# Kernel tuning notes

Hardware: AMD Instinct MI355X
Metric: run time of the kernel (lower is better)

The kernel has to match this reference:

```python
import jax, jax.numpy as jnp
import numpy as np

N_NODES = 10000
N_EDGES = 160000
F_IN, D1, D2, D_OUT, K = 512, 512, 512, 256, 3


def _gcn_layer(x, row, col, w, W, b, n):
    # PyG GCNConv (improved=False): add self-loops with weight 1, sym norm.
    loop = jnp.arange(n)
    r = jnp.concatenate([row, loop])
    c = jnp.concatenate([col, loop])
    ww = jnp.concatenate([w, jnp.ones((n,), w.dtype)])
    deg = jax.ops.segment_sum(ww, c, num_segments=n)
    dinv = jnp.where(deg > 0, jax.lax.rsqrt(deg), 0.0)
    norm = dinv[r] * ww * dinv[c]              # [E+N]
    h = x @ W                                  # dense GEMM first (as PyG lin)
    out = jax.ops.segment_sum(norm[:, None] * h[r], c, num_segments=n)
    return out + b


def _cheb_layer(x, row, col, w, Wk, b, n):
    # PyG ChebConv, normalization='sym', lambda_max=2.0:
    # L_hat = 2L/lmax - I = -D^{-1/2} A D^{-1/2} (self-loops removed first).
    w0 = jnp.where(row == col, jnp.zeros((), w.dtype), w)  # remove self loops
    deg = jax.ops.segment_sum(w0, row, num_segments=n)
    dinv = jnp.where(deg > 0, jax.lax.rsqrt(deg), 0.0)
    norm = dinv[row] * w0 * dinv[col]          # [E]

    def lhat(z):  # L_hat @ z
        return -jax.ops.segment_sum(norm[:, None] * z[row], col, num_segments=n)

    Tx0 = x
    out = Tx0 @ Wk[0]
    Tx1 = lhat(x)
    out = out + Tx1 @ Wk[1]
    for k in range(2, Wk.shape[0]):            # static K, fine to unroll
        Tx2 = 2.0 * lhat(Tx1) - Tx0
        out = out + Tx2 @ Wk[k]
        Tx0, Tx1 = Tx1, Tx2
    return out + b


def setup_inputs() -> dict:
    key = jax.random.key(0)
    ks = jax.random.split(key, 9)
    x = jax.random.normal(ks[0], (N_NODES, F_IN), dtype=jnp.float32)
    edge_index = jax.random.randint(ks[1], (2, N_EDGES), 0, N_NODES, dtype=jnp.int64)
    edge_weight = jax.random.uniform(ks[2], (N_EDGES,), dtype=jnp.float32)
    s = lambda fan: 1.0 / np.sqrt(fan)
    W1 = jax.random.normal(ks[3], (F_IN, D1), dtype=jnp.float32) * s(F_IN)
    b1 = jnp.zeros((D1,), jnp.float32)
    W2 = jax.random.normal(ks[4], (D1, D2), dtype=jnp.float32) * s(D1)
    b2 = jnp.zeros((D2,), jnp.float32)
    Wc = jax.random.normal(ks[5], (K, D2, D_OUT), dtype=jnp.float32) * s(D2)
    bc = jnp.zeros((D_OUT,), jnp.float32)
    return {"x": x, "edge_index": edge_index, "edge_weight": edge_weight,
            "W1": W1, "b1": b1, "W2": W2, "b2": b2, "Wc": Wc, "bc": bc}


def reference(x, edge_index, edge_weight, W1, b1, W2, b2, Wc, bc):
    row, col = edge_index[0], edge_index[1]
    n = x.shape[0]
    h = jax.nn.celu(_gcn_layer(x, row, col, edge_weight, W1, b1, n))
    h = jax.nn.celu(_gcn_layer(h, row, col, edge_weight, W2, b2, n))
    h = jax.nn.celu(_cheb_layer(h, row, col, edge_weight, Wc, bc, n))
    return h
```

## Files before the change

### kernel.cpp

```cpp
#include <hip/hip_runtime.h>
#include <math.h>

#define N_NODES 10000
#define N_EDGES 160000
#define FDIM    512
#define DOUT    256
#define NCAT    768

typedef unsigned short ushort_t;
typedef unsigned int   uint_t;
typedef __attribute__((ext_vector_type(8))) short bf16x8;
typedef __attribute__((ext_vector_type(4))) float f32x4;

__device__ inline ushort_t f2bf(float f) {
    uint_t u = __float_as_uint(f);
    u += 0x7fffu + ((u >> 16) & 1u);
    return (ushort_t)(u >> 16);
}
__device__ inline void bf2f8(uint4 u, float* v) {
    v[0] = __uint_as_float(u.x << 16); v[1] = __uint_as_float(u.x & 0xffff0000u);
    v[2] = __uint_as_float(u.y << 16); v[3] = __uint_as_float(u.y & 0xffff0000u);
    v[4] = __uint_as_float(u.z << 16); v[5] = __uint_as_float(u.z & 0xffff0000u);
    v[6] = __uint_as_float(u.w << 16); v[7] = __uint_as_float(u.w & 0xffff0000u);
}
__device__ inline uint4 f2bf8v(const float* v) {
    uint4 u;
    u.x = (uint_t)f2bf(v[0]) | ((uint_t)f2bf(v[1]) << 16);
    u.y = (uint_t)f2bf(v[2]) | ((uint_t)f2bf(v[3]) << 16);
    u.z = (uint_t)f2bf(v[4]) | ((uint_t)f2bf(v[5]) << 16);
    u.w = (uint_t)f2bf(v[6]) | ((uint_t)f2bf(v[7]) << 16);
    return u;
}
__device__ inline void gld_lds16(const ushort_t* g, ushort_t* l) {
    __builtin_amdgcn_global_load_lds(
        (const __attribute__((address_space(1))) unsigned int*)g,
        (__attribute__((address_space(3))) unsigned int*)l,
        16, 0, 0);
}

__global__ void k_edge_deg(const int* __restrict__ row, const int* __restrict__ col,
                           const float* __restrict__ w,
                           float* deg_g, float* deg_c, int* counts, int E) {
    int e = blockIdx.x * blockDim.x + threadIdx.x;
    if (e >= E) return;
    int r = row[e], c = col[e];
    float wv = w[e];
    atomicAdd(&deg_g[c], wv);
    if (r != c) atomicAdd(&deg_c[r], wv);
    atomicAdd(&counts[c], 1);
}

__global__ __launch_bounds__(256) void k_dinv_scan1(
    const float* __restrict__ deg_g, const float* __restrict__ deg_c,
    float* __restrict__ dinv_g, float* __restrict__ dinv_c,
    const int* __restrict__ counts, int* __restrict__ rp,
    int* __restrict__ part, int n)
{
    __shared__ int s[256];
    int tid = threadIdx.x;
    int i = blockIdx.x * 256 + tid;
    if (i < n) {
        dinv_g[i] = rsqrtf(deg_g[i] + 1.0f);
        float d = deg_c[i];
        dinv_c[i] = d > 0.f ? rsqrtf(d) : 0.f;
    }
    int v = (i < n) ? counts[i] : 0;
    s[tid] = v;
    __syncthreads();
    for (int o = 1; o < 256; o <<= 1) {
        int t = (tid >= o) ? s[tid - o] : 0;
        __syncthreads();
        s[tid] += t;
        __syncthreads();
    }
    if (i < n) rp[i] = s[tid] - v;
    if (tid == 255) part[blockIdx.x] = s[255];
}

__global__ __launch_bounds__(256) void k_scan23(int* __restrict__ rp,
                                                const int* __restrict__ part,
                                                int nb, int n) {
    __shared__ int soff[64];
    __shared__ int stot;
    int tid = threadIdx.x;
    if (tid < 64) {
        int v = (tid < nb) ? part[tid] : 0;
        int x = v;
        for (int o = 1; o < 64; o <<= 1) {
            int y = __shfl_up(x, o, 64);
            if (tid >= o) x += y;
        }
        soff[tid] = x - v;
        if (tid == 63) stot = x;
    }
    __syncthreads();
    int i = blockIdx.x * 256 + tid;
    if (i < n) rp[i] += soff[blockIdx.x];
    if (blockIdx.x == 0 && tid == 0) rp[n] = stot;
}

__global__ void k_fill(const int* __restrict__ row, const int* __restrict__ col,
                       const float* __restrict__ w,
                       const float* __restrict__ dinv_g, const float* __restrict__ dinv_c,
                       const int* __restrict__ rp, int* __restrict__ fill,
                       int2* __restrict__ eg, int2* __restrict__ ec, int E) {
    int e = blockIdx.x * blockDim.x + threadIdx.x;
    if (e >= E) return;
    int r = row[e], c = col[e];
    float wv = w[e];
    float ng = dinv_g[r] * wv * dinv_g[c];
    float w0 = (r == c) ? 0.f : wv;
    float nc = -(dinv_c[r] * w0 * dinv_c[c]);
    int pos = rp[c] + atomicAdd(&fill[c], 1);
    eg[pos] = make_int2(r, __float_as_int(ng));
    ec[pos] = make_int2(r, __float_as_int(nc));
}

#define XB_BLOCKS 5000

__global__ __launch_bounds__(256) void k_conv(
    const float* __restrict__ x,  ushort_t* __restrict__ xb,
    const float* __restrict__ W1, ushort_t* __restrict__ W1t,
    const float* __restrict__ W2, ushort_t* __restrict__ W2t,
    const float* __restrict__ Wc, ushort_t* __restrict__ Wcatt)
{
    int b = blockIdx.x;
    int tid = threadIdx.x;
    if (b < XB_BLOCKS) {
        int t = b * 256 + tid;
        float4 v = *(const float4*)(x + (size_t)t * 4);
        uint2 p;
        p.x = (uint_t)f2bf(v.x) | ((uint_t)f2bf(v.y) << 16);
        p.y = (uint_t)f2bf(v.z) | ((uint_t)f2bf(v.w) << 16);
        *(uint2*)(xb + (size_t)t * 4) = p;
        return;
    }
    b -= XB_BLOCKS;
    __shared__ float tile[64][65];
    const float* src; const float* src2 = nullptr;
    ushort_t* dst; int kt, ntG, srcld;
    if (b < 64) {
        kt = b >> 3; ntG = b & 7; srcld = FDIM;
        src = W1 + (size_t)(kt * 64) * FDIM + ntG * 64;
        dst = W1t;
    } else if (b < 128) {
        int bb = b - 64;
        kt = bb >> 3; ntG = bb & 7; srcld = FDIM;
        src = W2 + (size_t)(kt * 64) * FDIM + ntG * 64;
        dst = W2t;
    } else {
        int bb = b - 128;
        ntG = bb / 8; kt = bb % 8; srcld = DOUT;
        int s = ntG >> 2;
        int nl = (ntG & 3) * 64;
        if (s == 0) {
            src  = Wc + (size_t)(kt * 64) * DOUT + nl;
            src2 = Wc + (size_t)2 * FDIM * DOUT + (size_t)(kt * 64) * DOUT + nl;
        } else if (s == 1) {
            src  = Wc + (size_t)1 * FDIM * DOUT + (size_t)(kt * 64) * DOUT + nl;
        } else {
            src  = Wc + (size_t)2 * FDIM * DOUT + (size_t)(kt * 64) * DOUT + nl;
        }
        dst = Wcatt;
    }
    {
        int r = tid >> 2, c0 = (tid & 3) * 16;
        const float* sp = src + (size_t)r * srcld + c0;
#pragma unroll
        for (int q = 0; q < 4; ++q) {
            float4 a = *(const float4*)(sp + q * 4);
            if (src2) {
                float4 bsub = *(const float4*)(src2 + (size_t)r * srcld + c0 + q * 4);
                a.x -= bsub.x; a.y -= bsub.y; a.z -= bsub.z; a.w -= bsub.w;
            }
            tile[r][c0 + q * 4 + 0] = a.x;
            tile[r][c0 + q * 4 + 1] = a.y;
            tile[r][c0 + q * 4 + 2] = a.z;
            tile[r][c0 + q * 4 + 3] = a.w;
        }
    }
    __syncthreads();
    {
        int n = tid >> 2, k0 = (tid & 3) * 16;
        float v[16];
#pragma unroll
        for (int i = 0; i < 16; ++i) v[i] = tile[k0 + i][n];
        uint4 u0 = f2bf8v(v);
        uint4 u1 = f2bf8v(v + 8);
        ushort_t* dp = dst + (size_t)(ntG * 64 + n) * FDIM + kt * 64 + k0;
        *(uint4*)dp = u0;
        *(uint4*)(dp + 8) = u1;
    }
}

__global__ __launch_bounds__(256) void k_mgemm(
    const ushort_t* __restrict__ A, int lda,
    const ushort_t* __restrict__ Bt, int ldb,
    int M, int K, int N, int nbx, int nby,
    ushort_t* __restrict__ outB)
{
    __shared__ ushort_t As[128 * 32];
    __shared__ ushort_t Bs[128 * 32];

    int id = blockIdx.x;
    int j = id & 7, t = id >> 3;
    int by = t % nby;
    int bx = (t / nby) * 8 + j;
    if (bx >= nbx) return;

    const int tid  = threadIdx.x;
    const int w    = tid >> 6;
    const int lane = tid & 63;
    const int l15  = lane & 15;
    const int quad = lane >> 4;
    const int bm = bx * 128, bn = by * 128;
    const int wm = (w & 1) * 64;
    const int wn = (w >> 1) * 64;

    const int sr = lane >> 2;
    const int sc = (lane & 3) * 8;
    const ushort_t* ag[2]; ushort_t* al[2];
#pragma unroll
    for (int i = 0; i < 2; ++i) {
        int rt = (w * 2 + i) * 16 + sr;
        int ar = min(bm + rt, M - 1);
        ag[i] = A + (size_t)ar * lda + sc;
        al[i] = As + rt * 32 + sc;
    }
    const ushort_t* bg[2]; ushort_t* bl[2];
#pragma unroll
    for (int i = 0; i < 2; ++i) {
        int rt = (w * 2 + i) * 16 + sr;
        bg[i] = Bt + (size_t)(bn + rt) * ldb + sc;
        bl[i] = Bs + rt * 32 + sc;
    }

    f32x4 acc[4][4] = {};

    for (int k0 = 0; k0 < K; k0 += 32) {
        __syncthreads();
#pragma unroll
        for (int i = 0; i < 2; ++i) gld_lds16(ag[i] + k0, al[i]);
#pragma unroll
        for (int i = 0; i < 2; ++i) gld_lds16(bg[i] + k0, bl[i]);
        __syncthreads();
        bf16x8 af[4], bfr[4];
#pragma unroll
        for (int i = 0; i < 4; ++i)
            af[i] = *(const bf16x8*)(As + (wm + i * 16 + l15) * 32 + quad * 8);
#pragma unroll
        for (int jj = 0; jj < 4; ++jj)
            bfr[jj] = *(const bf16x8*)(Bs + (wn + jj * 16 + l15) * 32 + quad * 8);
#pragma unroll
        for (int i = 0; i < 4; ++i)
#pragma unroll
            for (int jj = 0; jj < 4; ++jj)
                acc[i][jj] = __builtin_amdgcn_mfma_f32_16x16x32_bf16(af[i], bfr[jj], acc[i][jj], 0, 0, 0);
    }

#pragma unroll
    for (int i = 0; i < 4; ++i) {
        int rowb = bm + wm + i * 16 + quad * 4;
#pragma unroll
        for (int jj = 0; jj < 4; ++jj) {
            int col = bn + wn + jj * 16 + l15;
#pragma unroll
            for (int r = 0; r < 4; ++r) {
                int rr = rowb + r;
                if (rr < M)
                    outB[(size_t)rr * N + col] = f2bf(acc[i][jj][r]);
            }
        }
    }
}

template<int SL>
__global__ __launch_bounds__(256) void k_sagg(
    const ushort_t* __restrict__ h, int hs, int hoff,
    const int2* __restrict__ er, const int* __restrict__ rp,
    const float* __restrict__ dinv_g,
    const ushort_t* __restrict__ other, int os, int ooff, float sB,
    const float* __restrict__ bias, float sA,
    ushort_t* __restrict__ outB, float* __restrict__ outF, int outs, int celu)
{
    const int id  = blockIdx.x;
    const int sl  = id % SL;
    const int tid = threadIdx.x;
    const int c   = (id / SL) * 32 + (tid >> 3);
    if (c >= N_NODES) return;
    const int f = sl * 64 + ((tid & 7) << 3);
    const ushort_t* hp = h + hoff + f;

    float acc[8] = {0.f, 0.f, 0.f, 0.f, 0.f, 0.f, 0.f, 0.f};
    int e = rp[c];
    const int e1 = rp[c + 1];
    for (; e + 2 <= e1; e += 2) {
        int2 p0 = er[e], p1 = er[e + 1];
        uint4 u0 = *(const uint4*)(hp + (size_t)p0.x * hs);
        uint4 u1 = *(const uint4*)(hp + (size_t)p1.x * hs);
        float n0 = __int_as_float(p0.y), n1 = __int_as_float(p1.y);
        float v0[8], v1[8];
        bf2f8(u0, v0); bf2f8(u1, v1);
#pragma unroll
        for (int i = 0; i < 8; ++i) {
            acc[i] = fmaf(n0, v0[i], acc[i]);
            acc[i] = fmaf(n1, v1[i], acc[i]);
        }
    }
    if (e < e1) {
        int2 p = er[e];
        uint4 u = *(const uint4*)(hp + (size_t)p.x * hs);
        float nv = __int_as_float(p.y);
        float v[8]; bf2f8(u, v);
#pragma unroll
        for (int i = 0; i < 8; ++i) acc[i] = fmaf(nv, v[i], acc[i]);
    }

    if (dinv_g) {
        float dv = dinv_g[c];
        float d2 = dv * dv;
        uint4 u = *(const uint4*)(hp + (size_t)c * hs);
        float v[8]; bf2f8(u, v);
#pragma unroll
        for (int i = 0; i < 8; ++i) acc[i] = fmaf(d2, v[i], acc[i]);
    }
    float r[8];
#pragma unroll
    for (int i = 0; i < 8; ++i) r[i] = sA * acc[i];
    if (other) {
        uint4 u = *(const uint4*)(other + (size_t)c * os + ooff + f);
        float o[8]; bf2f8(u, o);
#pragma unroll
        for (int i = 0; i < 8; ++i) r[i] = fmaf(sB, o[i], r[i]);
    }
    if (bias) {
#pragma unroll
        for (int i = 0; i < 8; ++i) r[i] += bias[f + i];
    }
    if (celu) {
#pragma unroll
        for (int i = 0; i < 8; ++i) r[i] = r[i] > 0.f ? r[i] : expm1f(r[i]);
    }
    if (outF) {
        float* op = outF + (size_t)c * outs + f;
        *(float4*)op       = make_float4(r[0], r[1], r[2], r[3]);
        *(float4*)(op + 4) = make_float4(r[4], r[5], r[6], r[7]);
    } else {
        *(uint4*)(outB + (size_t)c * outs + f) = f2bf8v(r);
    }
}


extern "C" void kernel_launch(void* const* d_in, const int* in_sizes, int n_in,
                              void* d_out, int out_size, void* d_ws, size_t ws_size,
                              hipStream_t stream) {
    const float* x  = (const float*)d_in[0];
    const int*   ei = (const int*)d_in[1];
    const float* ew = (const float*)d_in[2];
    const float* W1 = (const float*)d_in[3];
    const float* b1 = (const float*)d_in[4];
    const float* W2 = (const float*)d_in[5];
    const float* b2 = (const float*)d_in[6];
    const float* Wc = (const float*)d_in[7];
    const float* bc = (const float*)d_in[8];
    float* out = (float*)d_out;

    const int* row = ei;
    const int* col = ei + N_EDGES;

    char* ws = (char*)d_ws;
    size_t off = 0;
    auto alloc = [&](size_t bytes) -> void* {
        void* p = ws + off;
        off += (bytes + 255) & ~(size_t)255;
        return p;
    };
    ushort_t* xb    = (ushort_t*)alloc((size_t)N_NODES * FDIM * 2);
    ushort_t* bufA  = (ushort_t*)alloc((size_t)N_NODES * FDIM * 2);
    ushort_t* bufB  = (ushort_t*)alloc((size_t)N_NODES * FDIM * 2);
    ushort_t* Y     = (ushort_t*)alloc((size_t)N_NODES * NCAT * 2);
    ushort_t* P     = (ushort_t*)alloc((size_t)N_NODES * DOUT * 2);
    ushort_t* W1t   = (ushort_t*)alloc((size_t)FDIM * FDIM * 2);
    ushort_t* W2t   = (ushort_t*)alloc((size_t)FDIM * FDIM * 2);
    ushort_t* Wcatt = (ushort_t*)alloc((size_t)NCAT * FDIM * 2);
    size_t zs = off;
    float* deg_g  = (float*)alloc((size_t)N_NODES * 4);
    float* deg_c  = (float*)alloc((size_t)N_NODES * 4);
    int*   counts = (int*)alloc((size_t)N_NODES * 4);
    int*   fillb  = (int*)alloc((size_t)N_NODES * 4);
    size_t ze = off;
    float* dinv_g = (float*)alloc((size_t)N_NODES * 4);
    float* dinv_c = (float*)alloc((size_t)N_NODES * 4);
    int*   rp     = (int*)alloc((size_t)(N_NODES + 1) * 4);
    int*   part   = (int*)alloc(64 * 4);
    int2*  eg     = (int2*)alloc((size_t)N_EDGES * 8);
    int2*  ec     = (int2*)alloc((size_t)N_EDGES * 8);

    const int TB = 256;
    dim3 edgeGrid((N_EDGES + TB - 1) / TB);
    int nScanB = (N_NODES + 255) / 256;

    hipMemsetAsync(ws + zs, 0, ze - zs, stream);
    k_edge_deg<<<edgeGrid, TB, 0, stream>>>(row, col, ew, deg_g, deg_c, counts, N_EDGES);
    k_dinv_scan1<<<nScanB, 256, 0, stream>>>(deg_g, deg_c, dinv_g, dinv_c, counts, rp, part, N_NODES);
    k_scan23<<<nScanB, 256, 0, stream>>>(rp, part, nScanB, N_NODES);
    k_fill<<<edgeGrid, TB, 0, stream>>>(row, col, ew, dinv_g, dinv_c, rp, fillb, eg, ec, N_EDGES);

    k_conv<<<XB_BLOCKS + 224, 256, 0, stream>>>(x, xb, W1, W1t, W2, W2t, Wc, Wcatt);

    auto mgemm = [&](const ushort_t* A, const ushort_t* Bt, int N, ushort_t* oB) {
        int nbx = (N_NODES + 127) / 128, nby = N / 128;
        int G = 8 * (((nbx + 7) / 8) * nby);
        k_mgemm<<<G, 256, 0, stream>>>(A, FDIM, Bt, FDIM, N_NODES, FDIM, N, nbx, nby, oB);
    };
    int g8 = ((N_NODES + 31) / 32) * 8;
    int g4 = ((N_NODES + 31) / 32) * 4;

    mgemm(xb, W1t, FDIM, bufA);
    k_sagg<8><<<g8, 256, 0, stream>>>(bufA, FDIM, 0, eg, rp, dinv_g,
                                      (const ushort_t*)nullptr, 0, 0, 0.f,
                                      b1, 1.f, bufB, (float*)nullptr, FDIM, 1);
    mgemm(bufB, W2t, FDIM, bufA);
    k_sagg<8><<<g8, 256, 0, stream>>>(bufA, FDIM, 0, eg, rp, dinv_g,
                                      (const ushort_t*)nullptr, 0, 0, 0.f,
                                      b2, 1.f, bufB, (float*)nullptr, FDIM, 1);
    mgemm(bufB, Wcatt, NCAT, Y);
    k_sagg<4><<<g4, 256, 0, stream>>>(Y, NCAT, 2 * DOUT, ec, rp,
                                      (const float*)nullptr,
                                      Y, NCAT, DOUT, 1.f,
                                      (const float*)nullptr, 2.f,
                                      P, (float*)nullptr, DOUT, 0);
    k_sagg<4><<<g4, 256, 0, stream>>>(P, DOUT, 0, ec, rp,
                                      (const float*)nullptr,
                                      Y, NCAT, 0, 1.f,
                                      bc, 1.f,
                                      (ushort_t*)nullptr, out, DOUT, 1);
}
```

Baseline: 256.1 us.

## Fuse edge-degree with conversion kernel, shrink GEMM M-tile, unroll aggregation by four

The edge-degree atomics are merged into the bf16 conversion kernel, saving one launch and letting the two independent jobs overlap. The GEMM tile is reduced from 128x128 to 64x128 rows per block, which doubles the block count so the 10000-row problem fills more CUs, at the cost of less B-tile reuse. The sparse aggregation loop is unrolled to four edges per iteration to keep more gathers in flight, with a scalar remainder loop.

New measurement: 239.7 us, median of 3. 6.4% less time.

```diff
diff --git a/kernel.cpp b/kernel.cpp
--- a/kernel.cpp
+++ b/kernel.cpp
@@ -38,94 +38,33 @@
         16, 0, 0);
 }
 
-__global__ void k_edge_deg(const int* __restrict__ row, const int* __restrict__ col,
-                           const float* __restrict__ w,
-                           float* deg_g, float* deg_c, int* counts, int E) {
-    int e = blockIdx.x * blockDim.x + threadIdx.x;
-    if (e >= E) return;
-    int r = row[e], c = col[e];
-    float wv = w[e];
-    atomicAdd(&deg_g[c], wv);
-    if (r != c) atomicAdd(&deg_c[r], wv);
-    atomicAdd(&counts[c], 1);
-}
-
-__global__ __launch_bounds__(256) void k_dinv_scan1(
-    const float* __restrict__ deg_g, const float* __restrict__ deg_c,
-    float* __restrict__ dinv_g, float* __restrict__ dinv_c,
-    const int* __restrict__ counts, int* __restrict__ rp,
-    int* __restrict__ part, int n)
-{
-    __shared__ int s[256];
-    int tid = threadIdx.x;
-    int i = blockIdx.x * 256 + tid;
-    if (i < n) {
-        dinv_g[i] = rsqrtf(deg_g[i] + 1.0f);
-        float d = deg_c[i];
-        dinv_c[i] = d > 0.f ? rsqrtf(d) : 0.f;
-    }
-    int v = (i < n) ? counts[i] : 0;
-    s[tid] = v;
-    __syncthreads();
-    for (int o = 1; o < 256; o <<= 1) {
-        int t = (tid >= o) ? s[tid - o] : 0;
-        __syncthreads();
-        s[tid] += t;
-        __syncthreads();
-    }
-    if (i < n) rp[i] = s[tid] - v;
-    if (tid == 255) part[blockIdx.x] = s[255];
-}
-
-__global__ __launch_bounds__(256) void k_scan23(int* __restrict__ rp,
-                                                const int* __restrict__ part,
-                                                int nb, int n) {
-    __shared__ int soff[64];
-    __shared__ int stot;
-    int tid = threadIdx.x;
-    if (tid < 64) {
-        int v = (tid < nb) ? part[tid] : 0;
-        int x = v;
-        for (int o = 1; o < 64; o <<= 1) {
-            int y = __shfl_up(x, o, 64);
-            if (tid >= o) x += y;
-        }
-        soff[tid] = x - v;
-        if (tid == 63) stot = x;
-    }
-    __syncthreads();
-    int i = blockIdx.x * 256 + tid;
-    if (i < n) rp[i] += soff[blockIdx.x];
-    if (blockIdx.x == 0 && tid == 0) rp[n] = stot;
-}
-
-__global__ void k_fill(const int* __restrict__ row, const int* __restrict__ col,
-                       const float* __restrict__ w,
-                       const float* __restrict__ dinv_g, const float* __restrict__ dinv_c,
-                       const int* __restrict__ rp, int* __restrict__ fill,
-                       int2* __restrict__ eg, int2* __restrict__ ec, int E) {
-    int e = blockIdx.x * blockDim.x + threadIdx.x;
-    if (e >= E) return;
-    int r = row[e], c = col[e];
-    float wv = w[e];
-    float ng = dinv_g[r] * wv * dinv_g[c];
-    float w0 = (r == c) ? 0.f : wv;
-    float nc = -(dinv_c[r] * w0 * dinv_c[c]);
-    int pos = rp[c] + atomicAdd(&fill[c], 1);
-    eg[pos] = make_int2(r, __float_as_int(ng));
-    ec[pos] = make_int2(r, __float_as_int(nc));
-}
-
-#define XB_BLOCKS 5000
-
-__global__ __launch_bounds__(256) void k_conv(
+#define EDGE_BLOCKS 625
+#define XB_BLOCKS   5000
+
+__global__ __launch_bounds__(256) void k_pre1(
+    const int* __restrict__ row, const int* __restrict__ col,
+    const float* __restrict__ w,
+    float* deg_g, float* deg_c, int* counts,
     const float* __restrict__ x,  ushort_t* __restrict__ xb,
     const float* __restrict__ W1, ushort_t* __restrict__ W1t,
     const float* __restrict__ W2, ushort_t* __restrict__ W2t,
     const float* __restrict__ Wc, ushort_t* __restrict__ Wcatt)
 {
+    __shared__ float tile[64][65];
     int b = blockIdx.x;
     int tid = threadIdx.x;
+    if (b < EDGE_BLOCKS) {
+        int e = b * 256 + tid;
+        if (e < N_EDGES) {
+            int r = row[e], c = col[e];
+            float wv = w[e];
+            atomicAdd(&deg_g[c], wv);
+            if (r != c) atomicAdd(&deg_c[r], wv);
+            atomicAdd(&counts[c], 1);
+        }
+        return;
+    }
+    b -= EDGE_BLOCKS;
     if (b < XB_BLOCKS) {
         int t = b * 256 + tid;
         float4 v = *(const float4*)(x + (size_t)t * 4);
@@ -136,7 +75,6 @@
         return;
     }
     b -= XB_BLOCKS;
-    __shared__ float tile[64][65];
     const float* src; const float* src2 = nullptr;
     ushort_t* dst; int kt, ntG, srcld;
     if (b < 64) {
@@ -193,13 +131,79 @@
     }
 }
 
+__global__ __launch_bounds__(256) void k_dinv_scan1(
+    const float* __restrict__ deg_g, const float* __restrict__ deg_c,
+    float* __restrict__ dinv_g, float* __restrict__ dinv_c,
+    const int* __restrict__ counts, int* __restrict__ rp,
+    int* __restrict__ part, int n)
+{
+    __shared__ int s[256];
+    int tid = threadIdx.x;
+    int i = blockIdx.x * 256 + tid;
+    if (i < n) {
+        dinv_g[i] = rsqrtf(deg_g[i] + 1.0f);
+        float d = deg_c[i];
+        dinv_c[i] = d > 0.f ? rsqrtf(d) : 0.f;
+    }
+    int v = (i < n) ? counts[i] : 0;
+    s[tid] = v;
+    __syncthreads();
+    for (int o = 1; o < 256; o <<= 1) {
+        int t = (tid >= o) ? s[tid - o] : 0;
+        __syncthreads();
+        s[tid] += t;
+        __syncthreads();
+    }
+    if (i < n) rp[i] = s[tid] - v;
+    if (tid == 255) part[blockIdx.x] = s[255];
+}
+
+__global__ __launch_bounds__(256) void k_scan23(int* __restrict__ rp,
+                                                const int* __restrict__ part,
+                                                int nb, int n) {
+    __shared__ int soff[64];
+    __shared__ int stot;
+    int tid = threadIdx.x;
+    if (tid < 64) {
+        int v = (tid < nb) ? part[tid] : 0;
+        int x = v;
+        for (int o = 1; o < 64; o <<= 1) {
+            int y = __shfl_up(x, o, 64);
+            if (tid >= o) x += y;
+        }
+        soff[tid] = x - v;
+        if (tid == 63) stot = x;
+    }
+    __syncthreads();
+    int i = blockIdx.x * 256 + tid;
+    if (i < n) rp[i] += soff[blockIdx.x];
+    if (blockIdx.x == 0 && tid == 0) rp[n] = stot;
+}
+
+__global__ void k_fill(const int* __restrict__ row, const int* __restrict__ col,
+                       const float* __restrict__ w,
+                       const float* __restrict__ dinv_g, const float* __restrict__ dinv_c,
+                       const int* __restrict__ rp, int* __restrict__ fill,
+                       int2* __restrict__ eg, int2* __restrict__ ec, int E) {
+    int e = blockIdx.x * blockDim.x + threadIdx.x;
+    if (e >= E) return;
+    int r = row[e], c = col[e];
+    float wv = w[e];
+    float ng = dinv_g[r] * wv * dinv_g[c];
+    float w0 = (r == c) ? 0.f : wv;
+    float nc = -(dinv_c[r] * w0 * dinv_c[c]);
+    int pos = rp[c] + atomicAdd(&fill[c], 1);
+    eg[pos] = make_int2(r, __float_as_int(ng));
+    ec[pos] = make_int2(r, __float_as_int(nc));
+}
+
 __global__ __launch_bounds__(256) void k_mgemm(
     const ushort_t* __restrict__ A, int lda,
     const ushort_t* __restrict__ Bt, int ldb,
     int M, int K, int N, int nbx, int nby,
     ushort_t* __restrict__ outB)
 {
-    __shared__ ushort_t As[128 * 32];
+    __shared__ ushort_t As[64 * 32];
     __shared__ ushort_t Bs[128 * 32];
 
     int id = blockIdx.x;
@@ -213,53 +217,44 @@
     const int lane = tid & 63;
     const int l15  = lane & 15;
     const int quad = lane >> 4;
-    const int bm = bx * 128, bn = by * 128;
-    const int wm = (w & 1) * 64;
+    const int bm = bx * 64, bn = by * 128;
+    const int wm = (w & 1) * 32;
     const int wn = (w >> 1) * 64;
 
     const int sr = lane >> 2;
     const int sc = (lane & 3) * 8;
-    const ushort_t* ag[2]; ushort_t* al[2];
-#pragma unroll
-    for (int i = 0; i < 2; ++i) {
-        int rt = (w * 2 + i) * 16 + sr;
-        int ar = min(bm + rt, M - 1);
-        ag[i] = A + (size_t)ar * lda + sc;
-        al[i] = As + rt * 32 + sc;
-    }
-    const ushort_t* bg[2]; ushort_t* bl[2];
-#pragma unroll
-    for (int i = 0; i < 2; ++i) {
-        int rt = (w * 2 + i) * 16 + sr;
-        bg[i] = Bt + (size_t)(bn + rt) * ldb + sc;
-        bl[i] = Bs + rt * 32 + sc;
-    }
-
-    f32x4 acc[4][4] = {};
+    int arow = min(bm + w * 16 + sr, M - 1);
+    const ushort_t* ag = A + (size_t)arow * lda + sc;
+    ushort_t* al = As + (w * 16 + sr) * 32 + sc;
+    const ushort_t* bg0 = Bt + (size_t)(bn + w * 32 + sr) * ldb + sc;
+    const ushort_t* bg1 = bg0 + (size_t)16 * ldb;
+    ushort_t* bl0 = Bs + (w * 32 + sr) * 32 + sc;
+    ushort_t* bl1 = bl0 + 16 * 32;
+
+    f32x4 acc[2][4] = {};
 
     for (int k0 = 0; k0 < K; k0 += 32) {
         __syncthreads();
-#pragma unroll
-        for (int i = 0; i < 2; ++i) gld_lds16(ag[i] + k0, al[i]);
-#pragma unroll
-        for (int i = 0; i < 2; ++i) gld_lds16(bg[i] + k0, bl[i]);
+        gld_lds16(ag + k0, al);
+        gld_lds16(bg0 + k0, bl0);
+        gld_lds16(bg1 + k0, bl1);
         __syncthreads();
-        bf16x8 af[4], bfr[4];
-#pragma unroll
-        for (int i = 0; i < 4; ++i)
+        bf16x8 af[2], bfr[4];
+#pragma unroll
+        for (int i = 0; i < 2; ++i)
             af[i] = *(const bf16x8*)(As + (wm + i * 16 + l15) * 32 + quad * 8);
 #pragma unroll
         for (int jj = 0; jj < 4; ++jj)
             bfr[jj] = *(const bf16x8*)(Bs + (wn + jj * 16 + l15) * 32 + quad * 8);
 #pragma unroll
-        for (int i = 0; i < 4; ++i)
+        for (int i = 0; i < 2; ++i)
 #pragma unroll
             for (int jj = 0; jj < 4; ++jj)
                 acc[i][jj] = __builtin_amdgcn_mfma_f32_16x16x32_bf16(af[i], bfr[jj], acc[i][jj], 0, 0, 0);
     }
 
 #pragma unroll
-    for (int i = 0; i < 4; ++i) {
+    for (int i = 0; i < 2; ++i) {
         int rowb = bm + wm + i * 16 + quad * 4;
 #pragma unroll
         for (int jj = 0; jj < 4; ++jj) {
@@ -294,20 +289,25 @@
     float acc[8] = {0.f, 0.f, 0.f, 0.f, 0.f, 0.f, 0.f, 0.f};
     int e = rp[c];
     const int e1 = rp[c + 1];
-    for (; e + 2 <= e1; e += 2) {
-        int2 p0 = er[e], p1 = er[e + 1];
+    for (; e + 4 <= e1; e += 4) {
+        int2 p0 = er[e], p1 = er[e + 1], p2 = er[e + 2], p3 = er[e + 3];
         uint4 u0 = *(const uint4*)(hp + (size_t)p0.x * hs);
         uint4 u1 = *(const uint4*)(hp + (size_t)p1.x * hs);
+        uint4 u2 = *(const uint4*)(hp + (size_t)p2.x * hs);
+        uint4 u3 = *(const uint4*)(hp + (size_t)p3.x * hs);
         float n0 = __int_as_float(p0.y), n1 = __int_as_float(p1.y);
-        float v0[8], v1[8];
-        bf2f8(u0, v0); bf2f8(u1, v1);
+        float n2 = __int_as_float(p2.y), n3 = __int_as_float(p3.y);
+        float v0[8], v1[8], v2[8], v3[8];
+        bf2f8(u0, v0); bf2f8(u1, v1); bf2f8(u2, v2); bf2f8(u3, v3);
 #pragma unroll
         for (int i = 0; i < 8; ++i) {
             acc[i] = fmaf(n0, v0[i], acc[i]);
             acc[i] = fmaf(n1, v1[i], acc[i]);
-        }
-    }
-    if (e < e1) {
+            acc[i] = fmaf(n2, v2[i], acc[i]);
+            acc[i] = fmaf(n3, v3[i], acc[i]);
+        }
+    }
+    for (; e < e1; ++e) {
         int2 p = er[e];
         uint4 u = *(const uint4*)(hp + (size_t)p.x * hs);
         float nv = __int_as_float(p.y);
@@ -401,15 +401,15 @@
     int nScanB = (N_NODES + 255) / 256;
 
     hipMemsetAsync(ws + zs, 0, ze - zs, stream);
-    k_edge_deg<<<edgeGrid, TB, 0, stream>>>(row, col, ew, deg_g, deg_c, counts, N_EDGES);
+    k_pre1<<<EDGE_BLOCKS + XB_BLOCKS + 224, 256, 0, stream>>>(
+        row, col, ew, deg_g, deg_c, counts,
+        x, xb, W1, W1t, W2, W2t, Wc, Wcatt);
     k_dinv_scan1<<<nScanB, 256, 0, stream>>>(deg_g, deg_c, dinv_g, dinv_c, counts, rp, part, N_NODES);
     k_scan23<<<nScanB, 256, 0, stream>>>(rp, part, nScanB, N_NODES);
     k_fill<<<edgeGrid, TB, 0, stream>>>(row, col, ew, dinv_g, dinv_c, rp, fillb, eg, ec, N_EDGES);
 
-    k_conv<<<XB_BLOCKS + 224, 256, 0, stream>>>(x, xb, W1, W1t, W2, W2t, Wc, Wcatt);
-
     auto mgemm = [&](const ushort_t* A, const ushort_t* Bt, int N, ushort_t* oB) {
-        int nbx = (N_NODES + 127) / 128, nby = N / 128;
+        int nbx = (N_NODES + 63) / 64, nby = N / 128;
         int G = 8 * (((nbx + 7) / 8) * nby);
         k_mgemm<<<G, 256, 0, stream>>>(A, FDIM, Bt, FDIM, N_NODES, FDIM, N, nbx, nby, oB);
     };
```
